# Kernel tuning notes

Measured on AMD Instinct MI355X. Metric: run time of the kernel, lower is better.

The kernel has to match this reference:

```python
import jax, jax.numpy as jnp
import numpy as np
import math

INF = 10000000000.0
D_KEY = 128
SCALE = math.sqrt(D_KEY)


def setup_inputs() -> dict:
    key = jax.random.key(0)
    kq, kk, kv = jax.random.split(key, 3)
    B, S, D = 16, 2048, D_KEY
    return {
        "query": jax.random.normal(kq, (B, S, D), dtype=jnp.float32),
        "key": jax.random.normal(kk, (B, S, D), dtype=jnp.float32),
        "value": jax.random.normal(kv, (B, S, D), dtype=jnp.float32),
    }


def reference(query, key, value):
    # dot_products: [B, Sq, Sk]
    scores = jnp.einsum("bqd,bkd->bqk", query, key)
    S = key.shape[1]
    # NOTE: original subtracts the INF upper-triangular mask BEFORE dividing
    # by sqrt(d_key); replicate that order faithfully.
    tri = jnp.triu(jnp.full((S, S), INF, dtype=scores.dtype), k=1)
    scores = scores - tri[None, :, :]
    attn = jax.nn.softmax(scores / SCALE, axis=-1)
    # dropout with p=0.0 is identity
    return jnp.einsum("bqk,bkd->bqd", attn, value)
```

## Files before the change

kernel.cpp:

```cpp
#include <hip/hip_runtime.h>
#include <math.h>

#define S_LEN  2048
#define D_HEAD 128
#define QBLK   64
#define KVBLK  64
#define NWAVES 4
#define BATCH  16
#define NKVT   (S_LEN / KVBLK)
#define TILE_SH 8192

typedef __attribute__((ext_vector_type(4))) float f32x4;
typedef __attribute__((ext_vector_type(8))) short short8;

__device__ __forceinline__ unsigned short f2bf(float x) {
    union { float f; unsigned u; } v; v.f = x;
    unsigned r = v.u + 0x7fffu + ((v.u >> 16) & 1u);
    return (unsigned short)(r >> 16);
}
__device__ __forceinline__ unsigned pack2(unsigned short a, unsigned short b) {
    return (unsigned)a | ((unsigned)b << 16);
}
__device__ __forceinline__ unsigned cvtpk(float lo, float hi) {
    unsigned r;
    asm("v_cvt_pk_bf16_f32 %0, %1, %2" : "=v"(r) : "v"(lo), "v"(hi));
    return r;
}
__device__ __forceinline__ void gld16(const void* g, void* l) {
    __builtin_amdgcn_global_load_lds(
        (const __attribute__((address_space(1))) void*)g,
        (__attribute__((address_space(3))) void*)l, 16, 0, 0);
}
template<int N> __device__ __forceinline__ void wait_vm() {
    asm volatile("s_waitcnt vmcnt(%0)" :: "i"(N) : "memory");
}
__device__ __forceinline__ void barrier() {
    __builtin_amdgcn_sched_barrier(0);
    __builtin_amdgcn_s_barrier();
    __builtin_amdgcn_sched_barrier(0);
}

__global__ __launch_bounds__(256) void prep(const float* __restrict__ K,
                                            const float* __restrict__ V,
                                            unsigned short* __restrict__ Kp,
                                            unsigned short* __restrict__ Vp)
{
    const int tid = threadIdx.x;
    const int bid = blockIdx.x;
    const int b = bid >> 5, t = bid & 31;
    const size_t ibase = (size_t)b * S_LEN * D_HEAD + (size_t)t * KVBLK * D_HEAD;
    unsigned short* ko = Kp + (size_t)bid * TILE_SH;
    unsigned short* vo = Vp + (size_t)bid * TILE_SH;

    #pragma unroll
    for (int c = 0; c < 4; ++c) {
        int i  = c * 256 + tid;
        int k  = i >> 4;
        int d8 = ((i & 15) * 8) ^ ((k & 7) << 3);
        const float* sp = K + ibase + (size_t)k * D_HEAD + d8;
        float4 a = *(const float4*)sp;
        float4 bb = *(const float4*)(sp + 4);
        uint4 u = { pack2(f2bf(a.x),f2bf(a.y)),  pack2(f2bf(a.z),f2bf(a.w)),
                    pack2(f2bf(bb.x),f2bf(bb.y)),pack2(f2bf(bb.z),f2bf(bb.w)) };
        *(uint4*)(ko + i * 8) = u;
    }

    __shared__ unsigned short Vb[KVBLK][D_HEAD + 2];
    {
        const int r  = tid >> 2;
        const int c0 = (tid & 3) * 32;
        const float* sp = V + ibase + (size_t)r * D_HEAD + c0;
        #pragma unroll
        for (int i = 0; i < 8; ++i) {
            float4 x = *(const float4*)(sp + i * 4);
            Vb[r][c0+i*4+0] = f2bf(x.x); Vb[r][c0+i*4+1] = f2bf(x.y);
            Vb[r][c0+i*4+2] = f2bf(x.z); Vb[r][c0+i*4+3] = f2bf(x.w);
        }
    }
    __syncthreads();
    #pragma unroll
    for (int c = 0; c < 4; ++c) {
        int i   = c * 256 + tid;
        int d   = i >> 3;
        int kk0 = ((i & 7) * 8) ^ ((d & 7) << 3);
        unsigned short h[8];
        #pragma unroll
        for (int j = 0; j < 8; ++j) h[j] = Vb[kk0 + j][d];
        uint4 u = { pack2(h[0],h[1]), pack2(h[2],h[3]), pack2(h[4],h[5]), pack2(h[6],h[7]) };
        *(uint4*)(vo + i * 8) = u;
    }
}

template<int MODE>
__global__ __launch_bounds__(256, 4)
void attn_fwd(const float* __restrict__ Qg, const unsigned short* __restrict__ Kp,
              const unsigned short* __restrict__ Vp, float* __restrict__ Og,
              float* __restrict__ Po, float* __restrict__ Ml)
{
    constexpr float CSC = 0.12751744f;
    const int tid  = threadIdx.x;
    const int lane = tid & 63;
    const int w    = tid >> 6;
    const int bid  = blockIdx.x;

    int b, qb, lo_t, hi_t, pslot = -1;
    if (MODE == 0) {
        b = bid & 15;
        const int rank = bid >> 4;
        qb = (rank < 16) ? (31 - rank) : (rank - 16);
        lo_t = 0; hi_t = qb + 1;
    } else {
        const int r = bid >> 8;
        const int x = bid & 7;
        const int i = (bid >> 3) & 31;
        b = 2 * x + (i >> 4);
        const int a = i & 15;
        if (r < 2) {
            qb = 16 + a;
            const int h = (qb + 2) >> 1;
            lo_t = r ? h : 0;
            hi_t = r ? (qb + 1) : h;
            pslot = ((b << 4) | a) * 2 + r;
        } else {
            qb = 15 - a;
            lo_t = 0; hi_t = qb + 1;
        }
    }
    const int q0   = qb * QBLK;
    const int q0w  = q0 + w * 16;
    const int qc   = lane & 15;
    const int g    = lane >> 4;

    __shared__ __align__(16) unsigned short Klds[TILE_SH];
    __shared__ __align__(16) unsigned short Vlds[TILE_SH];
    __shared__ __align__(16) unsigned short Plds[NWAVES][16 * KVBLK];

    const size_t base = (size_t)b * S_LEN * D_HEAD;

    short8 qf[4];
    {
        const float* qp = Qg + base + (size_t)(q0w + qc) * D_HEAD + g * 8;
        #pragma unroll
        for (int db = 0; db < 4; ++db) {
            float4 x0 = *(const float4*)(qp + db * 32);
            float4 x1 = *(const float4*)(qp + db * 32 + 4);
            float tt[8] = {x0.x, x0.y, x0.z, x0.w, x1.x, x1.y, x1.z, x1.w};
            short8 f;
            #pragma unroll
            for (int j = 0; j < 8; ++j) f[j] = (short)f2bf(tt[j] * CSC);
            qf[db] = f;
        }
    }

    const int tb = b * NKVT;
    auto stage_K = [&](int t) {
        const unsigned short* ks = Kp + (size_t)(tb + t) * TILE_SH + w * 2048 + lane * 8;
        #pragma unroll
        for (int ii = 0; ii < 4; ++ii) gld16(ks + ii * 512, &Klds[w * 2048 + ii * 512]);
    };
    auto stage_V = [&](int t) {
        const unsigned short* vs = Vp + (size_t)(tb + t) * TILE_SH + w * 2048 + lane * 8;
        #pragma unroll
        for (int ii = 0; ii < 4; ++ii) gld16(vs + ii * 512, &Vlds[w * 2048 + ii * 512]);
    };

    f32x4 o[8] = {};
    float m = -1e30f, lsum = 0.f;
    const int qidx = q0w + qc;
    const int nt = hi_t - lo_t;

    stage_K(lo_t);
    stage_V(lo_t);

    for (int i = 0; i < nt; ++i) {
        const int t   = lo_t + i;
        const int kv0 = t * KVBLK;
        const bool more = (i + 1 < nt);

        wait_vm<4>();
        barrier();

        const int t16max = min(3, (q0w + 15 - kv0) >> 4);
        const int ksmax  = min(1, (q0w + 15 - kv0) >> 5);

        f32x4 st[4] = {};
        __builtin_amdgcn_s_setprio(1);
        #pragma unroll
        for (int t16 = 0; t16 < 4; ++t16) {
            if (t16 <= t16max) {
                const int kr = t16 * 16 + qc;
                const int swz = (kr & 7) << 3;
                #pragma unroll
                for (int db = 0; db < 4; ++db) {
                    short8 kf = *(const short8*)&Klds[(kr * 128 + db * 32 + g * 8) ^ swz];
                    st[t16] = __builtin_amdgcn_mfma_f32_16x16x32_bf16(kf, qf[db], st[t16], 0, 0, 0);
                }
            }
        }
        __builtin_amdgcn_s_setprio(0);

        barrier();
        if (more) stage_K(t + 1);

        float s[16];
        #pragma unroll
        for (int t16 = 0; t16 < 4; ++t16)
            #pragma unroll
            for (int r = 0; r < 4; ++r)
                s[t16*4+r] = (t16 <= t16max) ? st[t16][r] : -1e30f;

        if (kv0 + KVBLK - 1 > q0w) {
            #pragma unroll
            for (int t16 = 0; t16 < 4; ++t16)
                #pragma unroll
                for (int r = 0; r < 4; ++r)
                    if (kv0 + t16 * 16 + g * 4 + r > qidx) s[t16*4+r] = -1e30f;
        }

        float m0 = fmaxf(fmaxf(s[0],s[1]), fmaxf(s[2],s[3]));
        float m1 = fmaxf(fmaxf(s[4],s[5]), fmaxf(s[6],s[7]));
        float m2 = fmaxf(fmaxf(s[8],s[9]), fmaxf(s[10],s[11]));
        float m3 = fmaxf(fmaxf(s[12],s[13]), fmaxf(s[14],s[15]));
        float mx = fmaxf(fmaxf(m0,m1), fmaxf(m2,m3));

        if (__any(mx > m + 8.0f)) {
            mx = fmaxf(mx, __shfl_xor(mx, 16));
            mx = fmaxf(mx, __shfl_xor(mx, 32));
            float mnew = fmaxf(m, mx);
            float alpha = exp2f(m - mnew);
            m = mnew;
            lsum *= alpha;
            float a_o[4];
            #pragma unroll
            for (int r = 0; r < 4; ++r) a_o[r] = __shfl(alpha, g * 4 + r);
            #pragma unroll
            for (int db = 0; db < 8; ++db)
                #pragma unroll
                for (int r = 0; r < 4; ++r) o[db][r] *= a_o[r];
        }

        float p[16];
        #pragma unroll
        for (int ii = 0; ii < 16; ++ii) p[ii] = exp2f(s[ii] - m);
        float r0 = (p[0]+p[1]) + (p[2]+p[3]);
        float r1 = (p[4]+p[5]) + (p[6]+p[7]);
        float r2 = (p[8]+p[9]) + (p[10]+p[11]);
        float r3 = (p[12]+p[13]) + (p[14]+p[15]);
        lsum += (r0+r1) + (r2+r3);

        if (more) wait_vm<4>(); else wait_vm<0>();
        barrier();

        const int pswz = (qc & 7) << 3;
        #pragma unroll
        for (int t16 = 0; t16 < 4; ++t16) {
            uint2 u = { cvtpk(p[t16*4+0], p[t16*4+1]), cvtpk(p[t16*4+2], p[t16*4+3]) };
            *(uint2*)&Plds[w][(qc * 64 + t16 * 16 + g * 4) ^ pswz] = u;
        }

        __builtin_amdgcn_s_setprio(1);
        #pragma unroll
        for (int ks = 0; ks < 2; ++ks) {
            if (ks <= ksmax) {
                short8 pa = *(const short8*)&Plds[w][(qc * 64 + ks * 32 + g * 8) ^ pswz];
                #pragma unroll
                for (int db = 0; db < 8; ++db) {
                    const int d = db * 16 + qc;
                    short8 vf = *(const short8*)&Vlds[(d * 64 + ks * 32 + g * 8) ^ ((d & 7) << 3)];
                    o[db] = __builtin_amdgcn_mfma_f32_16x16x32_bf16(pa, vf, o[db], 0, 0, 0);
                }
            }
        }
        __builtin_amdgcn_s_setprio(0);

        barrier();
        if (more) stage_V(t + 1);
    }

    lsum += __shfl_xor(lsum, 16);
    lsum += __shfl_xor(lsum, 32);

    if (MODE == 1 && pslot >= 0) {
        float* po = Po + (size_t)pslot * (QBLK * D_HEAD);
        #pragma unroll
        for (int db = 0; db < 8; ++db)
            #pragma unroll
            for (int r = 0; r < 4; ++r)
                po[(w * 16 + g * 4 + r) * D_HEAD + db * 16 + qc] = o[db][r];
        if (g == 0) {
            float* ml = Ml + (size_t)pslot * (QBLK * 2);
            ml[(w * 16 + qc) * 2 + 0] = m;
            ml[(w * 16 + qc) * 2 + 1] = lsum;
        }
    } else {
        float linv = 1.0f / lsum;
        float li[4];
        #pragma unroll
        for (int r = 0; r < 4; ++r) li[r] = __shfl(linv, g * 4 + r);
        #pragma unroll
        for (int db = 0; db < 8; ++db)
            #pragma unroll
            for (int r = 0; r < 4; ++r)
                Og[base + (size_t)(q0w + g * 4 + r) * D_HEAD + db * 16 + qc] = o[db][r] * li[r];
    }
}

__global__ __launch_bounds__(256)
void combine(const float* __restrict__ Po, const float* __restrict__ Ml,
             float* __restrict__ Og)
{
    const int hq  = blockIdx.x;
    const int tid = threadIdx.x;
    const int b   = hq >> 4;
    const int qb  = 16 + (hq & 15);
    const int row = tid >> 2;
    const int c0  = (tid & 3) * 32;

    const float* mlA = Ml + (size_t)(hq * 2 + 0) * (QBLK * 2);
    const float* mlB = Ml + (size_t)(hq * 2 + 1) * (QBLK * 2);
    const float mA = mlA[row*2], lA = mlA[row*2+1];
    const float mB = mlB[row*2], lB = mlB[row*2+1];
    const float M  = fmaxf(mA, mB);
    const float aA = exp2f(mA - M), aB = exp2f(mB - M);
    const float rdenom = 1.0f / (aA * lA + aB * lB);

    const float* pA = Po + (size_t)(hq * 2 + 0) * (QBLK * D_HEAD) + row * D_HEAD + c0;
    const float* pB = Po + (size_t)(hq * 2 + 1) * (QBLK * D_HEAD) + row * D_HEAD + c0;
    float* op = Og + (size_t)b * S_LEN * D_HEAD + (size_t)(qb * QBLK + row) * D_HEAD + c0;

    #pragma unroll
    for (int j = 0; j < 8; ++j) {
        float4 xa = *(const float4*)(pA + j * 4);
        float4 xb = *(const float4*)(pB + j * 4);
        float4 r;
        r.x = (aA*xa.x + aB*xb.x) * rdenom;
        r.y = (aA*xa.y + aB*xb.y) * rdenom;
        r.z = (aA*xa.z + aB*xb.z) * rdenom;
        r.w = (aA*xa.w + aB*xb.w) * rdenom;
        *(float4*)(op + j * 4) = r;
    }
}

extern "C" void kernel_launch(void* const* d_in, const int* in_sizes, int n_in,
                              void* d_out, int out_size, void* d_ws, size_t ws_size,
                              hipStream_t stream) {
    const float* Q = (const float*)d_in[0];
    const float* K = (const float*)d_in[1];
    const float* V = (const float*)d_in[2];
    float* O = (float*)d_out;

    const size_t tile_elems = (size_t)BATCH * NKVT * TILE_SH;
    unsigned short* Kp = (unsigned short*)d_ws;
    unsigned short* Vp = Kp + tile_elems;
    float*          Po = (float*)(Vp + tile_elems);
    float*          Mlp = Po + (size_t)512 * QBLK * D_HEAD;
    const size_t need_bytes = (char*)(Mlp + 512 * QBLK * 2) - (char*)d_ws;

    prep<<<dim3(BATCH * NKVT), dim3(256), 0, stream>>>(K, V, Kp, Vp);
    if (ws_size >= need_bytes) {
        attn_fwd<1><<<dim3(768), dim3(256), 0, stream>>>(Q, Kp, Vp, O, Po, Mlp);
        combine<<<dim3(256), dim3(256), 0, stream>>>(Po, Mlp, O);
    } else {
        attn_fwd<0><<<dim3(512), dim3(256), 0, stream>>>(Q, Kp, Vp, O, nullptr, nullptr);
    }
}
```

Before: 64.15 us.

## Pair short causal query blocks per workgroup and store split partials in bf16

Changes the MODE 1 work split. Each of the first 128 workgroups now handles two short query blocks (qb and 15-qb) in sequence, with a direct epilogue in between. The 16 longest query blocks per batch are split in half across two workgroups. This drops the grid from 768 to 640 and evens out per-workgroup KV-tile counts. Split partial outputs are now written as bf16 instead of fp32, halving partial-buffer traffic in the combine kernel at some cost in precision.

Measured after the change: 71.05 us. 10.8% more time.

```diff
diff --git a/kernel.cpp b/kernel.cpp
--- a/kernel.cpp
+++ b/kernel.cpp
@@ -17,6 +17,10 @@
     union { float f; unsigned u; } v; v.f = x;
     unsigned r = v.u + 0x7fffu + ((v.u >> 16) & 1u);
     return (unsigned short)(r >> 16);
+}
+__device__ __forceinline__ float bf2f(unsigned short h) {
+    union { unsigned u; float f; } v; v.u = ((unsigned)h) << 16;
+    return v.f;
 }
 __device__ __forceinline__ unsigned pack2(unsigned short a, unsigned short b) {
     return (unsigned)a | ((unsigned)b << 16);
@@ -95,7 +99,7 @@
 __global__ __launch_bounds__(256, 4)
 void attn_fwd(const float* __restrict__ Qg, const unsigned short* __restrict__ Kp,
               const unsigned short* __restrict__ Vp, float* __restrict__ Og,
-              float* __restrict__ Po, float* __restrict__ Ml)
+              unsigned short* __restrict__ Po, float* __restrict__ Ml)
 {
     constexpr float CSC = 0.12751744f;
     const int tid  = threadIdx.x;
@@ -103,43 +107,42 @@
     const int w    = tid >> 6;
     const int bid  = blockIdx.x;
 
-    int b, qb, lo_t, hi_t, pslot = -1;
+    int b, qb0, lo0, n0, qb1 = -1, n1 = 0, pslot = -1;
     if (MODE == 0) {
         b = bid & 15;
         const int rank = bid >> 4;
-        qb = (rank < 16) ? (31 - rank) : (rank - 16);
-        lo_t = 0; hi_t = qb + 1;
+        qb0 = (rank < 16) ? (31 - rank) : (rank - 16);
+        lo0 = 0; n0 = qb0 + 1;
     } else {
-        const int r = bid >> 8;
-        const int x = bid & 7;
-        const int i = (bid >> 3) & 31;
-        b = 2 * x + (i >> 4);
-        const int a = i & 15;
-        if (r < 2) {
-            qb = 16 + a;
-            const int h = (qb + 2) >> 1;
-            lo_t = r ? h : 0;
-            hi_t = r ? (qb + 1) : h;
-            pslot = ((b << 4) | a) * 2 + r;
+        const int o = bid >> 4;
+        b = bid & 15;
+        if (o < 8) {
+            qb0 = o;      lo0 = 0; n0 = qb0 + 1;
+            qb1 = 15 - o; n1 = qb1 + 1;
         } else {
-            qb = 15 - a;
-            lo_t = 0; hi_t = qb + 1;
-        }
-    }
-    const int q0   = qb * QBLK;
-    const int q0w  = q0 + w * 16;
-    const int qc   = lane & 15;
-    const int g    = lane >> 4;
+            const int t = o - 8;
+            qb0 = 31 - (t >> 1);
+            const int n = qb0 + 1, h = (n + 1) >> 1, half = t & 1;
+            lo0 = half ? h : 0;
+            n0  = half ? (n - h) : h;
+            pslot = b * 32 + t;
+        }
+    }
+    const int nt = n0 + n1;
+    const int qc = lane & 15;
+    const int g  = lane >> 4;
 
     __shared__ __align__(16) unsigned short Klds[TILE_SH];
     __shared__ __align__(16) unsigned short Vlds[TILE_SH];
     __shared__ __align__(16) unsigned short Plds[NWAVES][16 * KVBLK];
 
     const size_t base = (size_t)b * S_LEN * D_HEAD;
+    const int tb = b * NKVT;
 
     short8 qf[4];
-    {
-        const float* qp = Qg + base + (size_t)(q0w + qc) * D_HEAD + g * 8;
+    auto load_q = [&](int qbx) {
+        const int q0wx = qbx * QBLK + w * 16;
+        const float* qp = Qg + base + (size_t)(q0wx + qc) * D_HEAD + g * 8;
         #pragma unroll
         for (int db = 0; db < 4; ++db) {
             float4 x0 = *(const float4*)(qp + db * 32);
@@ -150,9 +153,8 @@
             for (int j = 0; j < 8; ++j) f[j] = (short)f2bf(tt[j] * CSC);
             qf[db] = f;
         }
-    }
-
-    const int tb = b * NKVT;
+    };
+
     auto stage_K = [&](int t) {
         const unsigned short* ks = Kp + (size_t)(tb + t) * TILE_SH + w * 2048 + lane * 8;
         #pragma unroll
@@ -166,16 +168,36 @@
 
     f32x4 o[8] = {};
     float m = -1e30f, lsum = 0.f;
-    const int qidx = q0w + qc;
-    const int nt = hi_t - lo_t;
-
-    stage_K(lo_t);
-    stage_V(lo_t);
-
-    for (int i = 0; i < nt; ++i) {
-        const int t   = lo_t + i;
-        const int kv0 = t * KVBLK;
-        const bool more = (i + 1 < nt);
+
+    auto epi_direct = [&](int qbx) {
+        float ls = lsum;
+        ls += __shfl_xor(ls, 16);
+        ls += __shfl_xor(ls, 32);
+        float linv = 1.0f / ls;
+        float li[4];
+        #pragma unroll
+        for (int r = 0; r < 4; ++r) li[r] = __shfl(linv, g * 4 + r);
+        const int q0wx = qbx * QBLK + w * 16;
+        #pragma unroll
+        for (int db = 0; db < 8; ++db)
+            #pragma unroll
+            for (int r = 0; r < 4; ++r)
+                Og[base + (size_t)(q0wx + g * 4 + r) * D_HEAD + db * 16 + qc] = o[db][r] * li[r];
+    };
+
+    int qb_c = qb0;
+    int q0w  = qb_c * QBLK + w * 16;
+    int qidx = q0w + qc;
+
+    load_q(qb_c);
+    stage_K(lo0);
+    stage_V(lo0);
+
+    for (int u = 0; u < nt; ++u) {
+        const int t    = (u < n0) ? (lo0 + u) : (u - n0);
+        const int kv0  = t * KVBLK;
+        const bool more = (u + 1 < nt);
+        const int tnxt = more ? ((u + 1 < n0) ? (lo0 + u + 1) : (u + 1 - n0)) : 0;
 
         wait_vm<4>();
         barrier();
@@ -200,7 +222,7 @@
         __builtin_amdgcn_s_setprio(0);
 
         barrier();
-        if (more) stage_K(t + 1);
+        if (more) stage_K(tnxt);
 
         float s[16];
         #pragma unroll
@@ -254,8 +276,8 @@
         const int pswz = (qc & 7) << 3;
         #pragma unroll
         for (int t16 = 0; t16 < 4; ++t16) {
-            uint2 u = { cvtpk(p[t16*4+0], p[t16*4+1]), cvtpk(p[t16*4+2], p[t16*4+3]) };
-            *(uint2*)&Plds[w][(qc * 64 + t16 * 16 + g * 4) ^ pswz] = u;
+            uint2 uu = { cvtpk(p[t16*4+0], p[t16*4+1]), cvtpk(p[t16*4+2], p[t16*4+3]) };
+            *(uint2*)&Plds[w][(qc * 64 + t16 * 16 + g * 4) ^ pswz] = uu;
         }
 
         __builtin_amdgcn_s_setprio(1);
@@ -274,70 +296,83 @@
         __builtin_amdgcn_s_setprio(0);
 
         barrier();
-        if (more) stage_V(t + 1);
-    }
-
-    lsum += __shfl_xor(lsum, 16);
-    lsum += __shfl_xor(lsum, 32);
+        if (more) stage_V(tnxt);
+
+        if (MODE == 1 && n1 > 0 && u == n0 - 1) {
+            epi_direct(qb_c);
+            qb_c = qb1;
+            q0w  = qb_c * QBLK + w * 16;
+            qidx = q0w + qc;
+            load_q(qb_c);
+            #pragma unroll
+            for (int db = 0; db < 8; ++db) o[db] = (f32x4){0.f, 0.f, 0.f, 0.f};
+            m = -1e30f; lsum = 0.f;
+        }
+    }
 
     if (MODE == 1 && pslot >= 0) {
-        float* po = Po + (size_t)pslot * (QBLK * D_HEAD);
+        float ls = lsum;
+        ls += __shfl_xor(ls, 16);
+        ls += __shfl_xor(ls, 32);
+        unsigned short* po = Po + (size_t)pslot * (QBLK * D_HEAD);
         #pragma unroll
         for (int db = 0; db < 8; ++db)
             #pragma unroll
             for (int r = 0; r < 4; ++r)
-                po[(w * 16 + g * 4 + r) * D_HEAD + db * 16 + qc] = o[db][r];
+                po[(w * 16 + g * 4 + r) * D_HEAD + db * 16 + qc] = f2bf(o[db][r]);
         if (g == 0) {
             float* ml = Ml + (size_t)pslot * (QBLK * 2);
             ml[(w * 16 + qc) * 2 + 0] = m;
-            ml[(w * 16 + qc) * 2 + 1] = lsum;
+            ml[(w * 16 + qc) * 2 + 1] = ls;
         }
     } else {
-        float linv = 1.0f / lsum;
-        float li[4];
-        #pragma unroll
-        for (int r = 0; r < 4; ++r) li[r] = __shfl(linv, g * 4 + r);
-        #pragma unroll
-        for (int db = 0; db < 8; ++db)
-            #pragma unroll
-            for (int r = 0; r < 4; ++r)
-                Og[base + (size_t)(q0w + g * 4 + r) * D_HEAD + db * 16 + qc] = o[db][r] * li[r];
+        epi_direct(qb_c);
     }
 }
 
 __global__ __launch_bounds__(256)
-void combine(const float* __restrict__ Po, const float* __restrict__ Ml,
+void combine(const unsigned short* __restrict__ Po, const float* __restrict__ Ml,
              float* __restrict__ Og)
 {
-    const int hq  = blockIdx.x;
+    const int z   = blockIdx.x;
+    const int b   = z & 15;
+    const int qb  = 16 + (z >> 4);
     const int tid = threadIdx.x;
-    const int b   = hq >> 4;
-    const int qb  = 16 + (hq & 15);
     const int row = tid >> 2;
     const int c0  = (tid & 3) * 32;
 
-    const float* mlA = Ml + (size_t)(hq * 2 + 0) * (QBLK * 2);
-    const float* mlB = Ml + (size_t)(hq * 2 + 1) * (QBLK * 2);
+    const int pA = b * 32 + 2 * (31 - qb);
+    const int pB = pA + 1;
+
+    const float* mlA = Ml + (size_t)pA * (QBLK * 2);
+    const float* mlB = Ml + (size_t)pB * (QBLK * 2);
     const float mA = mlA[row*2], lA = mlA[row*2+1];
     const float mB = mlB[row*2], lB = mlB[row*2+1];
     const float M  = fmaxf(mA, mB);
     const float aA = exp2f(mA - M), aB = exp2f(mB - M);
-    const float rdenom = 1.0f / (aA * lA + aB * lB);
-
-    const float* pA = Po + (size_t)(hq * 2 + 0) * (QBLK * D_HEAD) + row * D_HEAD + c0;
-    const float* pB = Po + (size_t)(hq * 2 + 1) * (QBLK * D_HEAD) + row * D_HEAD + c0;
+    const float rd = 1.0f / (aA * lA + aB * lB);
+
+    const unsigned short* poA = Po + (size_t)pA * (QBLK * D_HEAD) + row * D_HEAD + c0;
+    const unsigned short* poB = Po + (size_t)pB * (QBLK * D_HEAD) + row * D_HEAD + c0;
     float* op = Og + (size_t)b * S_LEN * D_HEAD + (size_t)(qb * QBLK + row) * D_HEAD + c0;
 
     #pragma unroll
-    for (int j = 0; j < 8; ++j) {
-        float4 xa = *(const float4*)(pA + j * 4);
-        float4 xb = *(const float4*)(pB + j * 4);
-        float4 r;
-        r.x = (aA*xa.x + aB*xb.x) * rdenom;
-        r.y = (aA*xa.y + aB*xb.y) * rdenom;
-        r.z = (aA*xa.z + aB*xb.z) * rdenom;
-        r.w = (aA*xa.w + aB*xb.w) * rdenom;
-        *(float4*)(op + j * 4) = r;
+    for (int j = 0; j < 4; ++j) {
+        uint4 ua = *(const uint4*)(poA + j * 8);
+        uint4 ub = *(const uint4*)(poB + j * 8);
+        const unsigned short* ha = (const unsigned short*)&ua;
+        const unsigned short* hb = (const unsigned short*)&ub;
+        float4 o0, o1;
+        o0.x = (aA*bf2f(ha[0]) + aB*bf2f(hb[0])) * rd;
+        o0.y = (aA*bf2f(ha[1]) + aB*bf2f(hb[1])) * rd;
+        o0.z = (aA*bf2f(ha[2]) + aB*bf2f(hb[2])) * rd;
+        o0.w = (aA*bf2f(ha[3]) + aB*bf2f(hb[3])) * rd;
+        o1.x = (aA*bf2f(ha[4]) + aB*bf2f(hb[4])) * rd;
+        o1.y = (aA*bf2f(ha[5]) + aB*bf2f(hb[5])) * rd;
+        o1.z = (aA*bf2f(ha[6]) + aB*bf2f(hb[6])) * rd;
+        o1.w = (aA*bf2f(ha[7]) + aB*bf2f(hb[7])) * rd;
+        *(float4*)(op + j * 8)     = o0;
+        *(float4*)(op + j * 8 + 4) = o1;
     }
 }
 
@@ -352,13 +387,13 @@
     const size_t tile_elems = (size_t)BATCH * NKVT * TILE_SH;
     unsigned short* Kp = (unsigned short*)d_ws;
     unsigned short* Vp = Kp + tile_elems;
-    float*          Po = (float*)(Vp + tile_elems);
-    float*          Mlp = Po + (size_t)512 * QBLK * D_HEAD;
-    const size_t need_bytes = (char*)(Mlp + 512 * QBLK * 2) - (char*)d_ws;
+    unsigned short* Po = Vp + tile_elems;
+    float*          Mlp = (float*)(Po + (size_t)512 * QBLK * D_HEAD);
+    const size_t need_bytes = (char*)(Mlp + (size_t)512 * QBLK * 2) - (char*)d_ws;
 
     prep<<<dim3(BATCH * NKVT), dim3(256), 0, stream>>>(K, V, Kp, Vp);
     if (ws_size >= need_bytes) {
-        attn_fwd<1><<<dim3(768), dim3(256), 0, stream>>>(Q, Kp, Vp, O, Po, Mlp);
+        attn_fwd<1><<<dim3(640), dim3(256), 0, stream>>>(Q, Kp, Vp, O, Po, Mlp);
         combine<<<dim3(256), dim3(256), 0, stream>>>(Po, Mlp, O);
     } else {
         attn_fwd<0><<<dim3(512), dim3(256), 0, stream>>>(Q, Kp, Vp, O, nullptr, nullptr);
```

## Split long causal rows into up to three KV pieces with in-kernel atomic combine

Applied to the files above, without the earlier changes.

Changes the split-KV scheme from 768 blocks (the upper 16 query blocks split in two) to 1024 blocks, where query blocks 24-31 are split into three KV pieces, blocks 8-23 into two, and the rest run whole. The separate combine kernel is removed: the last piece to finish, detected with an atomic counter zeroed in the prep kernel, merges the partials in place. Partial outputs are stored in bf16 to halve workspace traffic. This aims to balance per-block work and remove a kernel launch, at the cost of threadfence and atomic overhead and some precision loss in the partial sums.

Result: slower. 238.0 us (+270.9%).

```diff
diff --git a/kernel.cpp b/kernel.cpp
--- a/kernel.cpp
+++ b/kernel.cpp
@@ -5,10 +5,10 @@
 #define D_HEAD 128
 #define QBLK   64
 #define KVBLK  64
-#define NWAVES 4
 #define BATCH  16
 #define NKVT   (S_LEN / KVBLK)
 #define TILE_SH 8192
+#define SLOTS_PB 56
 
 typedef __attribute__((ext_vector_type(4))) float f32x4;
 typedef __attribute__((ext_vector_type(8))) short short8;
@@ -18,6 +18,10 @@
     unsigned r = v.u + 0x7fffu + ((v.u >> 16) & 1u);
     return (unsigned short)(r >> 16);
 }
+__device__ __forceinline__ float bf2f(unsigned short h) {
+    union { unsigned u; float f; } v; v.u = ((unsigned)h) << 16;
+    return v.f;
+}
 __device__ __forceinline__ unsigned pack2(unsigned short a, unsigned short b) {
     return (unsigned)a | ((unsigned)b << 16);
 }
@@ -39,14 +43,19 @@
     __builtin_amdgcn_s_barrier();
     __builtin_amdgcn_sched_barrier(0);
 }
+__device__ __forceinline__ int slot_base(int b, int qb) {
+    return b * SLOTS_PB + ((qb >= 24) ? (32 + (qb - 24) * 3) : ((qb - 8) * 2));
+}
 
 __global__ __launch_bounds__(256) void prep(const float* __restrict__ K,
                                             const float* __restrict__ V,
                                             unsigned short* __restrict__ Kp,
-                                            unsigned short* __restrict__ Vp)
+                                            unsigned short* __restrict__ Vp,
+                                            int* __restrict__ Cnt)
 {
     const int tid = threadIdx.x;
     const int bid = blockIdx.x;
+    if (Cnt && bid == 0) { Cnt[tid] = 0; Cnt[tid + 256] = 0; }
     const int b = bid >> 5, t = bid & 31;
     const size_t ibase = (size_t)b * S_LEN * D_HEAD + (size_t)t * KVBLK * D_HEAD;
     unsigned short* ko = Kp + (size_t)bid * TILE_SH;
@@ -95,7 +104,8 @@
 __global__ __launch_bounds__(256, 4)
 void attn_fwd(const float* __restrict__ Qg, const unsigned short* __restrict__ Kp,
               const unsigned short* __restrict__ Vp, float* __restrict__ Og,
-              float* __restrict__ Po, float* __restrict__ Ml)
+              unsigned short* __restrict__ Po, float* __restrict__ Ml,
+              int* __restrict__ Cnt)
 {
     constexpr float CSC = 0.12751744f;
     const int tid  = threadIdx.x;
@@ -103,39 +113,47 @@
     const int w    = tid >> 6;
     const int bid  = blockIdx.x;
 
-    int b, qb, lo_t, hi_t, pslot = -1;
+    int b, qb, lo, nt, C = 1, piece = 0, pslot = -1;
     if (MODE == 0) {
         b = bid & 15;
         const int rank = bid >> 4;
         qb = (rank < 16) ? (31 - rank) : (rank - 16);
-        lo_t = 0; hi_t = qb + 1;
+        lo = 0; nt = qb + 1;
     } else {
-        const int r = bid >> 8;
-        const int x = bid & 7;
-        const int i = (bid >> 3) & 31;
-        b = 2 * x + (i >> 4);
-        const int a = i & 15;
-        if (r < 2) {
-            qb = 16 + a;
-            const int h = (qb + 2) >> 1;
-            lo_t = r ? h : 0;
-            hi_t = r ? (qb + 1) : h;
-            pslot = ((b << 4) | a) * 2 + r;
-        } else {
-            qb = 15 - a;
-            lo_t = 0; hi_t = qb + 1;
-        }
-    }
-    const int q0   = qb * QBLK;
-    const int q0w  = q0 + w * 16;
+        b = bid & 15;
+        const int o = bid >> 4, k = o & 15, r = o >> 4;
+        if (r <= 1)      { qb = 31 - k; C = (k < 8) ? 3 : 2; piece = r; }
+        else if (r == 2) { if (k < 8) { qb = 31 - k; C = 3; piece = 2; }
+                           else       { qb = k;      C = 2; piece = 0; } }
+        else             { if (k < 8) { qb = k;      C = 1; piece = 0; }
+                           else       { qb = k;      C = 2; piece = 1; } }
+        const int n = qb + 1, q_ = n / C, rem = n % C;
+        lo = piece * q_ + min(piece, rem);
+        nt = q_ + (piece < rem ? 1 : 0);
+        if (C > 1) pslot = slot_base(b, qb) + piece;
+    }
+    const int q0w  = qb * QBLK + w * 16;
     const int qc   = lane & 15;
     const int g    = lane >> 4;
+    const int qidx = q0w + qc;
 
     __shared__ __align__(16) unsigned short Klds[TILE_SH];
     __shared__ __align__(16) unsigned short Vlds[TILE_SH];
-    __shared__ __align__(16) unsigned short Plds[NWAVES][16 * KVBLK];
+    __shared__ __align__(16) unsigned short Plds[4][16 * KVBLK];
 
     const size_t base = (size_t)b * S_LEN * D_HEAD;
+    const int tb = b * NKVT;
+
+    auto stage_K = [&](int t) {
+        const unsigned short* ks = Kp + (size_t)(tb + t) * TILE_SH + w * 2048 + lane * 8;
+        #pragma unroll
+        for (int ii = 0; ii < 4; ++ii) gld16(ks + ii * 512, &Klds[w * 2048 + ii * 512]);
+    };
+    auto stage_V = [&](int t) {
+        const unsigned short* vs = Vp + (size_t)(tb + t) * TILE_SH + w * 2048 + lane * 8;
+        #pragma unroll
+        for (int ii = 0; ii < 4; ++ii) gld16(vs + ii * 512, &Vlds[w * 2048 + ii * 512]);
+    };
 
     short8 qf[4];
     {
@@ -147,33 +165,19 @@
             float tt[8] = {x0.x, x0.y, x0.z, x0.w, x1.x, x1.y, x1.z, x1.w};
             short8 f;
             #pragma unroll
-            for (int j = 0; j < 8; ++j) f[j] = (short)f2bf(tt[j] * CSC);
+            for (int jj = 0; jj < 8; ++jj) f[jj] = (short)f2bf(tt[jj] * CSC);
             qf[db] = f;
         }
     }
 
-    const int tb = b * NKVT;
-    auto stage_K = [&](int t) {
-        const unsigned short* ks = Kp + (size_t)(tb + t) * TILE_SH + w * 2048 + lane * 8;
-        #pragma unroll
-        for (int ii = 0; ii < 4; ++ii) gld16(ks + ii * 512, &Klds[w * 2048 + ii * 512]);
-    };
-    auto stage_V = [&](int t) {
-        const unsigned short* vs = Vp + (size_t)(tb + t) * TILE_SH + w * 2048 + lane * 8;
-        #pragma unroll
-        for (int ii = 0; ii < 4; ++ii) gld16(vs + ii * 512, &Vlds[w * 2048 + ii * 512]);
-    };
-
-    f32x4 o[8] = {};
+    f32x4 acc[8] = {};
     float m = -1e30f, lsum = 0.f;
-    const int qidx = q0w + qc;
-    const int nt = hi_t - lo_t;
-
-    stage_K(lo_t);
-    stage_V(lo_t);
+
+    stage_K(lo);
+    stage_V(lo);
 
     for (int i = 0; i < nt; ++i) {
-        const int t   = lo_t + i;
+        const int t   = lo + i;
         const int kv0 = t * KVBLK;
         const bool more = (i + 1 < nt);
 
@@ -236,16 +240,16 @@
             #pragma unroll
             for (int db = 0; db < 8; ++db)
                 #pragma unroll
-                for (int r = 0; r < 4; ++r) o[db][r] *= a_o[r];
-        }
-
-        float p[16];
-        #pragma unroll
-        for (int ii = 0; ii < 16; ++ii) p[ii] = exp2f(s[ii] - m);
-        float r0 = (p[0]+p[1]) + (p[2]+p[3]);
-        float r1 = (p[4]+p[5]) + (p[6]+p[7]);
-        float r2 = (p[8]+p[9]) + (p[10]+p[11]);
-        float r3 = (p[12]+p[13]) + (p[14]+p[15]);
+                for (int r = 0; r < 4; ++r) acc[db][r] *= a_o[r];
+        }
+
+        float p16[16];
+        #pragma unroll
+        for (int ii = 0; ii < 16; ++ii) p16[ii] = exp2f(s[ii] - m);
+        float r0 = (p16[0]+p16[1]) + (p16[2]+p16[3]);
+        float r1 = (p16[4]+p16[5]) + (p16[6]+p16[7]);
+        float r2 = (p16[8]+p16[9]) + (p16[10]+p16[11]);
+        float r3 = (p16[12]+p16[13]) + (p16[14]+p16[15]);
         lsum += (r0+r1) + (r2+r3);
 
         if (more) wait_vm<4>(); else wait_vm<0>();
@@ -254,8 +258,8 @@
         const int pswz = (qc & 7) << 3;
         #pragma unroll
         for (int t16 = 0; t16 < 4; ++t16) {
-            uint2 u = { cvtpk(p[t16*4+0], p[t16*4+1]), cvtpk(p[t16*4+2], p[t16*4+3]) };
-            *(uint2*)&Plds[w][(qc * 64 + t16 * 16 + g * 4) ^ pswz] = u;
+            uint2 uu = { cvtpk(p16[t16*4+0], p16[t16*4+1]), cvtpk(p16[t16*4+2], p16[t16*4+3]) };
+            *(uint2*)&Plds[w][(qc * 64 + t16 * 16 + g * 4) ^ pswz] = uu;
         }
 
         __builtin_amdgcn_s_setprio(1);
@@ -267,7 +271,7 @@
                 for (int db = 0; db < 8; ++db) {
                     const int d = db * 16 + qc;
                     short8 vf = *(const short8*)&Vlds[(d * 64 + ks * 32 + g * 8) ^ ((d & 7) << 3)];
-                    o[db] = __builtin_amdgcn_mfma_f32_16x16x32_bf16(pa, vf, o[db], 0, 0, 0);
+                    acc[db] = __builtin_amdgcn_mfma_f32_16x16x32_bf16(pa, vf, acc[db], 0, 0, 0);
                 }
             }
         }
@@ -280,63 +284,78 @@
     lsum += __shfl_xor(lsum, 16);
     lsum += __shfl_xor(lsum, 32);
 
-    if (MODE == 1 && pslot >= 0) {
-        float* po = Po + (size_t)pslot * (QBLK * D_HEAD);
+    if (pslot < 0) {
+        float linv = 1.0f / lsum;
+        float li[4];
+        #pragma unroll
+        for (int r = 0; r < 4; ++r) li[r] = __shfl(linv, g * 4 + r);
         #pragma unroll
         for (int db = 0; db < 8; ++db)
             #pragma unroll
             for (int r = 0; r < 4; ++r)
-                po[(w * 16 + g * 4 + r) * D_HEAD + db * 16 + qc] = o[db][r];
+                Og[base + (size_t)(q0w + g * 4 + r) * D_HEAD + db * 16 + qc] = acc[db][r] * li[r];
+        return;
+    }
+
+    {
+        unsigned short* po = Po + (size_t)pslot * (QBLK * D_HEAD);
+        #pragma unroll
+        for (int db = 0; db < 8; ++db)
+            #pragma unroll
+            for (int r = 0; r < 4; ++r)
+                po[(w * 16 + g * 4 + r) * D_HEAD + db * 16 + qc] = f2bf(acc[db][r]);
         if (g == 0) {
             float* ml = Ml + (size_t)pslot * (QBLK * 2);
             ml[(w * 16 + qc) * 2 + 0] = m;
             ml[(w * 16 + qc) * 2 + 1] = lsum;
         }
-    } else {
-        float linv = 1.0f / lsum;
-        float li[4];
-        #pragma unroll
-        for (int r = 0; r < 4; ++r) li[r] = __shfl(linv, g * 4 + r);
-        #pragma unroll
-        for (int db = 0; db < 8; ++db)
-            #pragma unroll
-            for (int r = 0; r < 4; ++r)
-                Og[base + (size_t)(q0w + g * 4 + r) * D_HEAD + db * 16 + qc] = o[db][r] * li[r];
-    }
-}
-
-__global__ __launch_bounds__(256)
-void combine(const float* __restrict__ Po, const float* __restrict__ Ml,
-             float* __restrict__ Og)
-{
-    const int hq  = blockIdx.x;
-    const int tid = threadIdx.x;
-    const int b   = hq >> 4;
-    const int qb  = 16 + (hq & 15);
-    const int row = tid >> 2;
-    const int c0  = (tid & 3) * 32;
-
-    const float* mlA = Ml + (size_t)(hq * 2 + 0) * (QBLK * 2);
-    const float* mlB = Ml + (size_t)(hq * 2 + 1) * (QBLK * 2);
-    const float mA = mlA[row*2], lA = mlA[row*2+1];
-    const float mB = mlB[row*2], lB = mlB[row*2+1];
-    const float M  = fmaxf(mA, mB);
-    const float aA = exp2f(mA - M), aB = exp2f(mB - M);
-    const float rdenom = 1.0f / (aA * lA + aB * lB);
-
-    const float* pA = Po + (size_t)(hq * 2 + 0) * (QBLK * D_HEAD) + row * D_HEAD + c0;
-    const float* pB = Po + (size_t)(hq * 2 + 1) * (QBLK * D_HEAD) + row * D_HEAD + c0;
-    float* op = Og + (size_t)b * S_LEN * D_HEAD + (size_t)(qb * QBLK + row) * D_HEAD + c0;
-
+    }
+    __threadfence();
+    __syncthreads();
+    if (tid == 0) ((int*)Plds)[0] = atomicAdd(&Cnt[b * 32 + qb], 1);
+    __syncthreads();
+    if (((int*)Plds)[0] != C - 1) return;
+
+    __threadfence();
+    const int row = tid >> 2, c0 = (tid & 3) * 32;
+    const int sb  = slot_base(b, qb);
+    float mm[3], lv[3], M = -1e30f;
+    #pragma unroll
+    for (int c = 0; c < 3; ++c) {
+        if (c < C) {
+            const float* ml = Ml + (size_t)(sb + c) * (QBLK * 2);
+            mm[c] = ml[row * 2 + 0];
+            lv[c] = ml[row * 2 + 1];
+            M = fmaxf(M, mm[c]);
+        }
+    }
+    float den = 0.f, wgt[3];
+    #pragma unroll
+    for (int c = 0; c < 3; ++c) {
+        if (c < C) { wgt[c] = exp2f(mm[c] - M); den += wgt[c] * lv[c]; }
+    }
+    const float rd = 1.0f / den;
+    float am[32];
+    #pragma unroll
+    for (int j = 0; j < 32; ++j) am[j] = 0.f;
+    #pragma unroll
+    for (int c = 0; c < 3; ++c) {
+        if (c < C) {
+            const unsigned short* po = Po + (size_t)(sb + c) * (QBLK * D_HEAD) + row * D_HEAD + c0;
+            const float wc = wgt[c];
+            #pragma unroll
+            for (int j = 0; j < 4; ++j) {
+                uint4 u = *(const uint4*)(po + j * 8);
+                const unsigned short* h = (const unsigned short*)&u;
+                #pragma unroll
+                for (int e = 0; e < 8; ++e) am[j * 8 + e] += wc * bf2f(h[e]);
+            }
+        }
+    }
+    float* op = Og + base + (size_t)(qb * QBLK + row) * D_HEAD + c0;
     #pragma unroll
     for (int j = 0; j < 8; ++j) {
-        float4 xa = *(const float4*)(pA + j * 4);
-        float4 xb = *(const float4*)(pB + j * 4);
-        float4 r;
-        r.x = (aA*xa.x + aB*xb.x) * rdenom;
-        r.y = (aA*xa.y + aB*xb.y) * rdenom;
-        r.z = (aA*xa.z + aB*xb.z) * rdenom;
-        r.w = (aA*xa.w + aB*xb.w) * rdenom;
+        float4 r = { am[j*4+0] * rd, am[j*4+1] * rd, am[j*4+2] * rd, am[j*4+3] * rd };
         *(float4*)(op + j * 4) = r;
     }
 }
@@ -350,17 +369,19 @@
     float* O = (float*)d_out;
 
     const size_t tile_elems = (size_t)BATCH * NKVT * TILE_SH;
+    const size_t nslots = (size_t)BATCH * SLOTS_PB;
     unsigned short* Kp = (unsigned short*)d_ws;
     unsigned short* Vp = Kp + tile_elems;
-    float*          Po = (float*)(Vp + tile_elems);
-    float*          Mlp = Po + (size_t)512 * QBLK * D_HEAD;
-    const size_t need_bytes = (char*)(Mlp + 512 * QBLK * 2) - (char*)d_ws;
-
-    prep<<<dim3(BATCH * NKVT), dim3(256), 0, stream>>>(K, V, Kp, Vp);
+    unsigned short* Po = Vp + tile_elems;
+    float*          Mlp = (float*)(Po + nslots * QBLK * D_HEAD);
+    int*            Cnt = (int*)(Mlp + nslots * QBLK * 2);
+    const size_t need_bytes = (char*)(Cnt + 512) - (char*)d_ws;
+
     if (ws_size >= need_bytes) {
-        attn_fwd<1><<<dim3(768), dim3(256), 0, stream>>>(Q, Kp, Vp, O, Po, Mlp);
-        combine<<<dim3(256), dim3(256), 0, stream>>>(Po, Mlp, O);
+        prep<<<dim3(BATCH * NKVT), dim3(256), 0, stream>>>(K, V, Kp, Vp, Cnt);
+        attn_fwd<1><<<dim3(1024), dim3(256), 0, stream>>>(Q, Kp, Vp, O, Po, Mlp, Cnt);
     } else {
-        attn_fwd<0><<<dim3(512), dim3(256), 0, stream>>>(Q, Kp, Vp, O, nullptr, nullptr);
-    }
-}
+        prep<<<dim3(BATCH * NKVT), dim3(256), 0, stream>>>(K, V, Kp, Vp, nullptr);
+        attn_fwd<0><<<dim3(512), dim3(256), 0, stream>>>(Q, Kp, Vp, O, nullptr, nullptr, nullptr);
+    }
+}
```
